# Optimization experiments

Measured on AMD Instinct MI355X. Metric: run time of the kernel, lower is better.

Reference implementation:

```python
import jax, jax.numpy as jnp
import numpy as np

BN_EPS = 1e-5


def setup_inputs() -> dict:
    key = jax.random.key(0)
    ks = jax.random.split(key, 10)
    B, C, N = 16, 512, 4096
    Cr = C // 4
    s = 0.05
    return {
        "x": jax.random.normal(ks[0], (B, C, N), dtype=jnp.float32),
        # channel attention MLP (1x1 convs on pooled vector)
        "w1": jax.random.normal(ks[1], (Cr, C), dtype=jnp.float32) * s,
        "b1": jnp.zeros((Cr,), jnp.float32),
        "w2": jax.random.normal(ks[2], (C, Cr), dtype=jnp.float32) * s,
        "b2": jnp.zeros((C,), jnp.float32),
        # spatial attention branch
        "w3": jax.random.normal(ks[3], (Cr, C), dtype=jnp.float32) * s,
        "b3": jnp.zeros((Cr,), jnp.float32),
        "bn_gamma": jnp.ones((Cr,), jnp.float32),
        "bn_beta": jnp.zeros((Cr,), jnp.float32),
        "bn_mean": jnp.zeros((Cr,), jnp.float32),
        "bn_var": jnp.ones((Cr,), jnp.float32),
        "w4": jax.random.normal(ks[4], (1, Cr), dtype=jnp.float32) * s,
        "b4": jnp.zeros((1,), jnp.float32),
    }


def reference(x, w1, b1, w2, b2, w3, b3, bn_gamma, bn_beta, bn_mean, bn_var, w4, b4):
    # x: [B, C, N]; inference semantics (Dropout = identity, BN uses running stats)
    # ---- channel attention ----
    pooled = jnp.mean(x, axis=-1)                        # [B, C] (AdaptiveAvgPool1d(1))
    h = jax.nn.relu(pooled @ w1.T + b1)                  # [B, C/4]
    ca = jax.nn.sigmoid(h @ w2.T + b2)[:, :, None]       # [B, C, 1]
    x_ca = x * ca                                        # [B, C, N]
    # ---- spatial attention ----
    h2 = jnp.einsum('oc,bcn->bon', w3, x_ca) + b3[:, None]    # [B, C/4, N]
    inv = bn_gamma / jnp.sqrt(bn_var + BN_EPS)                 # [C/4]
    h2 = h2 * inv[:, None] + (bn_beta - bn_mean * inv)[:, None]
    h2 = jax.nn.relu(h2)
    sa = jax.nn.sigmoid(jnp.einsum('oc,bcn->bon', w4, h2) + b4[:, None])  # [B, 1, N]
    return x + x_ca * sa
```

## Files before the change

### kernel.cpp

```cpp
#include <hip/hip_runtime.h>
#include <math.h>

constexpr int B  = 16;
constexpr int C  = 512;
constexpr int N  = 4096;
constexpr int CR = 128;
constexpr int NT = 64;
constexpr int KC = 64;

typedef __attribute__((ext_vector_type(8))) short bf16x8;
typedef __attribute__((ext_vector_type(4))) float f32x4;

__device__ __forceinline__ float sigmoidf_(float v) {
    return 1.0f / (1.0f + __expf(-v));
}
__device__ __forceinline__ unsigned short f2bf(float f) {
    unsigned u = __float_as_uint(f);
    u += 0x7fffu + ((u >> 16) & 1u);
    return (unsigned short)(u >> 16);
}

__global__ __launch_bounds__(256) void k_prep(
    const float* __restrict__ w3, const float* __restrict__ b3,
    const float* __restrict__ gamma, const float* __restrict__ beta,
    const float* __restrict__ mean, const float* __restrict__ var,
    unsigned short* __restrict__ w3s, float* __restrict__ bias2)
{
    int idx = blockIdx.x * 256 + threadIdx.x;
    int o  = idx >> 6;
    int g  = idx & 63;
    int ck = g >> 3;
    int c8 = (g & 7) * 8;
    int c  = ck * KC + c8;
    float inv = gamma[o] * rsqrtf(var[o] + 1e-5f);
    float4 a = *(const float4*)(w3 + o * C + c);
    float4 bq = *(const float4*)(w3 + o * C + c + 4);
    unsigned r0 = (unsigned)f2bf(a.x * inv) | ((unsigned)f2bf(a.y * inv) << 16);
    unsigned r1 = (unsigned)f2bf(a.z * inv) | ((unsigned)f2bf(a.w * inv) << 16);
    unsigned r2 = (unsigned)f2bf(bq.x * inv) | ((unsigned)f2bf(bq.y * inv) << 16);
    unsigned r3 = (unsigned)f2bf(bq.z * inv) | ((unsigned)f2bf(bq.w * inv) << 16);
    int byte = (o * 128 + c8 * 2) ^ ((o & 7) << 4);
    *(uint4*)((char*)w3s + ck * 16384 + byte) = make_uint4(r0, r1, r2, r3);
    if (idx < CR) {
        float iv = gamma[idx] * rsqrtf(var[idx] + 1e-5f);
        bias2[idx] = b3[idx] * iv + beta[idx] - mean[idx] * iv;
    }
}

__global__ __launch_bounds__(256) void k_pool(
    const float* __restrict__ x, float* __restrict__ pooled)
{
    int w    = threadIdx.x >> 6;
    int lane = threadIdx.x & 63;
    int row  = blockIdx.x * 4 + w;
    const float4* xr = (const float4*)(x + (size_t)row * N);
    float s = 0.f;
    #pragma unroll
    for (int i = 0; i < 16; ++i) {
        float4 v = xr[i * 64 + lane];
        s += v.x + v.y + v.z + v.w;
    }
    #pragma unroll
    for (int off = 32; off; off >>= 1) s += __shfl_xor(s, off, 64);
    if (lane == 0) pooled[row] = s * (1.0f / N);
}

__global__ __launch_bounds__(128) void k_ca(
    const float* __restrict__ pooled,
    const float* __restrict__ w1, const float* __restrict__ b1,
    const float* __restrict__ w2, const float* __restrict__ b2,
    float* __restrict__ ca)
{
    __shared__ float ps[C];
    __shared__ float hs[CR];
    int b = blockIdx.x, t = threadIdx.x;
    #pragma unroll
    for (int i = 0; i < 4; ++i) ps[t + i * 128] = pooled[b * C + t + i * 128];
    __syncthreads();

    float acc = b1[t];
    const float4* wr = (const float4*)(w1 + t * C);
    const float4* pr = (const float4*)ps;
    #pragma unroll 4
    for (int i = 0; i < C / 4; ++i) {
        float4 wv = wr[i], pv = pr[i];
        acc += wv.x * pv.x + wv.y * pv.y + wv.z * pv.z + wv.w * pv.w;
    }
    hs[t] = fmaxf(acc, 0.f);
    __syncthreads();

    #pragma unroll
    for (int k = 0; k < 4; ++k) {
        int c2 = t + k * 128;
        float a = b2[c2];
        const float4* w2r = (const float4*)(w2 + c2 * CR);
        const float4* hr  = (const float4*)hs;
        #pragma unroll 4
        for (int i = 0; i < CR / 4; ++i) {
            float4 wv = w2r[i], hv = hr[i];
            a += wv.x * hv.x + wv.y * hv.y + wv.z * hv.z + wv.w * hv.w;
        }
        ca[b * C + c2] = sigmoidf_(a);
    }
}

__global__ __launch_bounds__(256) void k_main(
    const float* __restrict__ x, const float* __restrict__ ca,
    const unsigned short* __restrict__ w3s, const float* __restrict__ bias2,
    const float* __restrict__ w4, const float* __restrict__ b4,
    float* __restrict__ out)
{
    __shared__ __align__(16) short lds_w[CR * KC];
    __shared__ __align__(16) short lds_x[NT * KC];
    __shared__ float ca_s[C];
    __shared__ __align__(16) float sa_s[NT];
    __shared__ float red[2][NT];
    __shared__ float bias2_s[CR];
    __shared__ float w4_s[CR];

    const int t    = threadIdx.x;
    const int lane = t & 63;
    const int w    = t >> 6;
    const int b    = blockIdx.y;
    const int n0   = blockIdx.x * NT;
    const int wo   = (w & 1) * 64;
    const int wn   = (w >> 1) * 32;

    ca_s[t]       = ca[b * C + t];
    ca_s[t + 256] = ca[b * C + t + 256];
    if (t < CR) { bias2_s[t] = bias2[t]; w4_s[t] = w4[t]; }

    const size_t xbase = (size_t)b * C * N + n0;

    f32x4 acc[4][2];
    #pragma unroll
    for (int i = 0; i < 4; ++i) { acc[i][0] = (f32x4)0.f; acc[i][1] = (f32x4)0.f; }

    const int ng = t & 31;
    const int cg = t >> 5;

    for (int ck = 0; ck < C / KC; ++ck) {
        const int c0 = ck * KC;
        __syncthreads();
        const char* wsrc = (const char*)w3s + ck * 16384;
        #pragma unroll
        for (int i = 0; i < 4; ++i)
            *(uint4*)((char*)lds_w + i * 4096 + t * 16) =
                *(const uint4*)(wsrc + i * 4096 + t * 16);
        {
            float2 v[8];
            #pragma unroll
            for (int ci = 0; ci < 8; ++ci)
                v[ci] = *(const float2*)(x + xbase + (size_t)(c0 + cg * 8 + ci) * N + 2 * ng);
            unsigned q0[4], q1[4];
            #pragma unroll
            for (int h = 0; h < 4; ++h) {
                float s0 = ca_s[c0 + cg * 8 + 2 * h];
                float s1 = ca_s[c0 + cg * 8 + 2 * h + 1];
                q0[h] = (unsigned)f2bf(v[2 * h].x * s0) | ((unsigned)f2bf(v[2 * h + 1].x * s1) << 16);
                q1[h] = (unsigned)f2bf(v[2 * h].y * s0) | ((unsigned)f2bf(v[2 * h + 1].y * s1) << 16);
            }
            int nl0 = 2 * ng, nl1 = 2 * ng + 1;
            int a0 = (nl0 * 128 + cg * 16) ^ ((nl0 & 7) << 4);
            int a1 = (nl1 * 128 + cg * 16) ^ ((nl1 & 7) << 4);
            *(uint4*)((char*)lds_x + a0) = make_uint4(q0[0], q0[1], q0[2], q0[3]);
            *(uint4*)((char*)lds_x + a1) = make_uint4(q1[0], q1[1], q1[2], q1[3]);
        }
        __syncthreads();
        #pragma unroll
        for (int kk = 0; kk < 2; ++kk) {
            bf16x8 af[4], bfr[2];
            #pragma unroll
            for (int i = 0; i < 4; ++i) {
                int ar = wo + i * 16 + (lane & 15);
                int ab = (ar * 128 + kk * 64 + (lane >> 4) * 16) ^ ((ar & 7) << 4);
                af[i] = *(const bf16x8*)((const char*)lds_w + ab);
            }
            #pragma unroll
            for (int j = 0; j < 2; ++j) {
                int br = wn + j * 16 + (lane & 15);
                int bb = (br * 128 + kk * 64 + (lane >> 4) * 16) ^ ((br & 7) << 4);
                bfr[j] = *(const bf16x8*)((const char*)lds_x + bb);
            }
            #pragma unroll
            for (int i = 0; i < 4; ++i)
                #pragma unroll
                for (int j = 0; j < 2; ++j)
                    acc[i][j] = __builtin_amdgcn_mfma_f32_16x16x32_bf16(af[i], bfr[j], acc[i][j], 0, 0, 0);
        }
    }

    #pragma unroll
    for (int j = 0; j < 2; ++j) {
        float p = 0.f;
        #pragma unroll
        for (int i = 0; i < 4; ++i) {
            #pragma unroll
            for (int r = 0; r < 4; ++r) {
                int o = wo + i * 16 + (lane >> 4) * 4 + r;
                float hval = acc[i][j][r] + bias2_s[o];
                p = fmaf(w4_s[o], fmaxf(hval, 0.f), p);
            }
        }
        p += __shfl_xor(p, 16, 64);
        p += __shfl_xor(p, 32, 64);
        if (lane < 16) red[w & 1][wn + j * 16 + lane] = p;
    }
    __syncthreads();
    if (t < NT) sa_s[t] = sigmoidf_(red[0][t] + red[1][t] + b4[0]);
    __syncthreads();

    #pragma unroll 4
    for (int it = 0; it < 32; ++it) {
        int f4 = it * 256 + t;
        int c  = f4 >> 4;
        int n4 = f4 & 15;
        size_t off = xbase + (size_t)c * N + n4 * 4;
        float4 v = *(const float4*)(x + off);
        float cav = ca_s[c];
        float4 sv = *(const float4*)&sa_s[n4 * 4];
        float4 o4;
        o4.x = v.x * fmaf(cav, sv.x, 1.0f);
        o4.y = v.y * fmaf(cav, sv.y, 1.0f);
        o4.z = v.z * fmaf(cav, sv.z, 1.0f);
        o4.w = v.w * fmaf(cav, sv.w, 1.0f);
        *(float4*)(out + off) = o4;
    }
}

extern "C" void kernel_launch(void* const* d_in, const int* in_sizes, int n_in,
                              void* d_out, int out_size, void* d_ws, size_t ws_size,
                              hipStream_t stream)
{
    const float* x   = (const float*)d_in[0];
    const float* w1  = (const float*)d_in[1];
    const float* b1  = (const float*)d_in[2];
    const float* w2  = (const float*)d_in[3];
    const float* b2  = (const float*)d_in[4];
    const float* w3  = (const float*)d_in[5];
    const float* b3  = (const float*)d_in[6];
    const float* g   = (const float*)d_in[7];
    const float* be  = (const float*)d_in[8];
    const float* mn  = (const float*)d_in[9];
    const float* vr  = (const float*)d_in[10];
    const float* w4  = (const float*)d_in[11];
    const float* b4  = (const float*)d_in[12];
    float* out = (float*)d_out;

    float* ws     = (float*)d_ws;
    float* pooled = ws;
    float* ca     = ws + 8192;
    float* bias2  = ws + 16384;
    unsigned short* w3s = (unsigned short*)(ws + 16640);

    k_prep<<<32, 256, 0, stream>>>(w3, b3, g, be, mn, vr, w3s, bias2);
    k_pool<<<B * C / 4, 256, 0, stream>>>(x, pooled);
    k_ca<<<B, 128, 0, stream>>>(pooled, w1, b1, w2, b2, ca);
    dim3 g3(N / NT, B);
    k_main<<<g3, 256, 0, stream>>>(x, ca, w3s, bias2, w4, b4, out);
}
```

Measured before the change: 126.6 us.

## Prefetch next chunk into registers in main loop and merge prep/pool kernels

The main GEMM loop now issues global loads of x and the packed weights for the next channel chunk before computing the current one. It also replaces __syncthreads with barriers that wait only on LDS counters, so the global loads overlap the MFMA work. Separately, the weight-prep and pooling kernels are merged into one launch to save launch overhead. The prefetch buffers raise register pressure and may reduce occupancy.

```diff
diff --git a/kernel.cpp b/kernel.cpp
--- a/kernel.cpp
+++ b/kernel.cpp
@@ -14,55 +14,60 @@
 __device__ __forceinline__ float sigmoidf_(float v) {
     return 1.0f / (1.0f + __expf(-v));
 }
-__device__ __forceinline__ unsigned short f2bf(float f) {
+__device__ __forceinline__ unsigned f2bf(float f) {
     unsigned u = __float_as_uint(f);
     u += 0x7fffu + ((u >> 16) & 1u);
-    return (unsigned short)(u >> 16);
-}
-
-__global__ __launch_bounds__(256) void k_prep(
+    return u >> 16;
+}
+
+#define LGKM_BARRIER() do {                                   \
+    asm volatile("s_waitcnt lgkmcnt(0)" ::: "memory");        \
+    __builtin_amdgcn_s_barrier();                             \
+    asm volatile("" ::: "memory");                            \
+} while (0)
+
+__global__ __launch_bounds__(256) void k_pre(
+    const float* __restrict__ x, float* __restrict__ pooled,
     const float* __restrict__ w3, const float* __restrict__ b3,
     const float* __restrict__ gamma, const float* __restrict__ beta,
     const float* __restrict__ mean, const float* __restrict__ var,
     unsigned short* __restrict__ w3s, float* __restrict__ bias2)
 {
-    int idx = blockIdx.x * 256 + threadIdx.x;
-    int o  = idx >> 6;
-    int g  = idx & 63;
-    int ck = g >> 3;
-    int c8 = (g & 7) * 8;
-    int c  = ck * KC + c8;
-    float inv = gamma[o] * rsqrtf(var[o] + 1e-5f);
-    float4 a = *(const float4*)(w3 + o * C + c);
-    float4 bq = *(const float4*)(w3 + o * C + c + 4);
-    unsigned r0 = (unsigned)f2bf(a.x * inv) | ((unsigned)f2bf(a.y * inv) << 16);
-    unsigned r1 = (unsigned)f2bf(a.z * inv) | ((unsigned)f2bf(a.w * inv) << 16);
-    unsigned r2 = (unsigned)f2bf(bq.x * inv) | ((unsigned)f2bf(bq.y * inv) << 16);
-    unsigned r3 = (unsigned)f2bf(bq.z * inv) | ((unsigned)f2bf(bq.w * inv) << 16);
-    int byte = (o * 128 + c8 * 2) ^ ((o & 7) << 4);
-    *(uint4*)((char*)w3s + ck * 16384 + byte) = make_uint4(r0, r1, r2, r3);
-    if (idx < CR) {
-        float iv = gamma[idx] * rsqrtf(var[idx] + 1e-5f);
-        bias2[idx] = b3[idx] * iv + beta[idx] - mean[idx] * iv;
-    }
-}
-
-__global__ __launch_bounds__(256) void k_pool(
-    const float* __restrict__ x, float* __restrict__ pooled)
-{
-    int w    = threadIdx.x >> 6;
-    int lane = threadIdx.x & 63;
-    int row  = blockIdx.x * 4 + w;
-    const float4* xr = (const float4*)(x + (size_t)row * N);
-    float s = 0.f;
-    #pragma unroll
-    for (int i = 0; i < 16; ++i) {
-        float4 v = xr[i * 64 + lane];
-        s += v.x + v.y + v.z + v.w;
-    }
-    #pragma unroll
-    for (int off = 32; off; off >>= 1) s += __shfl_xor(s, off, 64);
-    if (lane == 0) pooled[row] = s * (1.0f / N);
+    if (blockIdx.x < 2048) {
+        int w    = threadIdx.x >> 6;
+        int lane = threadIdx.x & 63;
+        int row  = blockIdx.x * 4 + w;
+        const float4* xr = (const float4*)(x + (size_t)row * N);
+        float s = 0.f;
+        #pragma unroll
+        for (int i = 0; i < 16; ++i) {
+            float4 v = xr[i * 64 + lane];
+            s += v.x + v.y + v.z + v.w;
+        }
+        #pragma unroll
+        for (int off = 32; off; off >>= 1) s += __shfl_xor(s, off, 64);
+        if (lane == 0) pooled[row] = s * (1.0f / N);
+    } else {
+        int idx = (blockIdx.x - 2048) * 256 + threadIdx.x;
+        int o  = idx >> 6;
+        int g  = idx & 63;
+        int ck = g >> 3;
+        int c8 = (g & 7) * 8;
+        int c  = ck * KC + c8;
+        float inv = gamma[o] * rsqrtf(var[o] + 1e-5f);
+        float4 a  = *(const float4*)(w3 + o * C + c);
+        float4 bq = *(const float4*)(w3 + o * C + c + 4);
+        unsigned r0 = f2bf(a.x * inv)  | (f2bf(a.y * inv) << 16);
+        unsigned r1 = f2bf(a.z * inv)  | (f2bf(a.w * inv) << 16);
+        unsigned r2 = f2bf(bq.x * inv) | (f2bf(bq.y * inv) << 16);
+        unsigned r3 = f2bf(bq.z * inv) | (f2bf(bq.w * inv) << 16);
+        int byte = (o * 128 + c8 * 2) ^ ((o & 7) << 4);
+        *(uint4*)((char*)w3s + ck * 16384 + byte) = make_uint4(r0, r1, r2, r3);
+        if (idx < CR) {
+            float iv = gamma[idx] * rsqrtf(var[idx] + 1e-5f);
+            bias2[idx] = b3[idx] * iv + beta[idx] - mean[idx] * iv;
+        }
+    }
 }
 
 __global__ __launch_bounds__(128) void k_ca(
@@ -131,34 +136,42 @@
     if (t < CR) { bias2_s[t] = bias2[t]; w4_s[t] = w4[t]; }
 
     const size_t xbase = (size_t)b * C * N + n0;
-
-    f32x4 acc[4][2];
-    #pragma unroll
-    for (int i = 0; i < 4; ++i) { acc[i][0] = (f32x4)0.f; acc[i][1] = (f32x4)0.f; }
-
     const int ng = t & 31;
     const int cg = t >> 5;
 
+    float2 xv[8];
+    uint4  wv[4];
+
+#define LOADX(CK) do { const int c0_ = (CK) * KC;                              \
+    _Pragma("unroll") for (int ci = 0; ci < 8; ++ci)                           \
+        xv[ci] = *(const float2*)(x + xbase + (size_t)(c0_ + cg * 8 + ci) * N + 2 * ng); \
+} while (0)
+#define LOADW(CK) do { const char* ws_ = (const char*)w3s + (CK) * 16384;      \
+    _Pragma("unroll") for (int i = 0; i < 4; ++i)                              \
+        wv[i] = *(const uint4*)(ws_ + i * 4096 + t * 16);                      \
+} while (0)
+
+    f32x4 acc[4][2];
+    #pragma unroll
+    for (int i = 0; i < 4; ++i) { acc[i][0] = (f32x4)0.f; acc[i][1] = (f32x4)0.f; }
+
+    LOADX(0);
+    LOADW(0);
+    LGKM_BARRIER();
+
     for (int ck = 0; ck < C / KC; ++ck) {
         const int c0 = ck * KC;
-        __syncthreads();
-        const char* wsrc = (const char*)w3s + ck * 16384;
         #pragma unroll
         for (int i = 0; i < 4; ++i)
-            *(uint4*)((char*)lds_w + i * 4096 + t * 16) =
-                *(const uint4*)(wsrc + i * 4096 + t * 16);
+            *(uint4*)((char*)lds_w + i * 4096 + t * 16) = wv[i];
         {
-            float2 v[8];
-            #pragma unroll
-            for (int ci = 0; ci < 8; ++ci)
-                v[ci] = *(const float2*)(x + xbase + (size_t)(c0 + cg * 8 + ci) * N + 2 * ng);
             unsigned q0[4], q1[4];
             #pragma unroll
             for (int h = 0; h < 4; ++h) {
                 float s0 = ca_s[c0 + cg * 8 + 2 * h];
                 float s1 = ca_s[c0 + cg * 8 + 2 * h + 1];
-                q0[h] = (unsigned)f2bf(v[2 * h].x * s0) | ((unsigned)f2bf(v[2 * h + 1].x * s1) << 16);
-                q1[h] = (unsigned)f2bf(v[2 * h].y * s0) | ((unsigned)f2bf(v[2 * h + 1].y * s1) << 16);
+                q0[h] = f2bf(xv[2 * h].x * s0) | (f2bf(xv[2 * h + 1].x * s1) << 16);
+                q1[h] = f2bf(xv[2 * h].y * s0) | (f2bf(xv[2 * h + 1].y * s1) << 16);
             }
             int nl0 = 2 * ng, nl1 = 2 * ng + 1;
             int a0 = (nl0 * 128 + cg * 16) ^ ((nl0 & 7) << 4);
@@ -166,7 +179,11 @@
             *(uint4*)((char*)lds_x + a0) = make_uint4(q0[0], q0[1], q0[2], q0[3]);
             *(uint4*)((char*)lds_x + a1) = make_uint4(q1[0], q1[1], q1[2], q1[3]);
         }
-        __syncthreads();
+        if (ck < C / KC - 1) {
+            LOADX(ck + 1);
+            LOADW(ck + 1);
+        }
+        LGKM_BARRIER();
         #pragma unroll
         for (int kk = 0; kk < 2; ++kk) {
             bf16x8 af[4], bfr[2];
@@ -188,6 +205,7 @@
                 for (int j = 0; j < 2; ++j)
                     acc[i][j] = __builtin_amdgcn_mfma_f32_16x16x32_bf16(af[i], bfr[j], acc[i][j], 0, 0, 0);
         }
+        LGKM_BARRIER();
     }
 
     #pragma unroll
@@ -226,6 +244,8 @@
         o4.w = v.w * fmaf(cav, sv.w, 1.0f);
         *(float4*)(out + off) = o4;
     }
+#undef LOADX
+#undef LOADW
 }
 
 extern "C" void kernel_launch(void* const* d_in, const int* in_sizes, int n_in,
@@ -253,8 +273,7 @@
     float* bias2  = ws + 16384;
     unsigned short* w3s = (unsigned short*)(ws + 16640);
 
-    k_prep<<<32, 256, 0, stream>>>(w3, b3, g, be, mn, vr, w3s, bias2);
-    k_pool<<<B * C / 4, 256, 0, stream>>>(x, pooled);
+    k_pre<<<2048 + 32, 256, 0, stream>>>(x, pooled, w3, b3, g, be, mn, vr, w3s, bias2);
     k_ca<<<B, 128, 0, stream>>>(pooled, w1, b1, w2, b2, ca);
     dim3 g3(N / NT, B);
     k_main<<<g3, 256, 0, stream>>>(x, ca, w3s, bias2, w4, b4, out);
```

After: 141.0 us. 11.4% more time.
